# Optimization experiments

Measured on AMD Instinct MI355X. Metric: run time of the kernel, lower is better.

The kernel has to match this reference:

```python
import jax, jax.numpy as jnp
import numpy as np


def _sample_level(tables, gx, gy, align_corners):
    # tables: [3, C, H, W]; gx, gy: [3, P] grid coords in [-1, 1]
    # emulates F.grid_sample(mode='bilinear', padding_mode='border')
    def one(tab, x, y):
        C, H, W = tab.shape
        if align_corners:
            ix = (x + 1.0) * 0.5 * (W - 1)
            iy = (y + 1.0) * 0.5 * (H - 1)
        else:
            ix = ((x + 1.0) * W - 1.0) * 0.5
            iy = ((y + 1.0) * H - 1.0) * 0.5
        ix = jnp.clip(ix, 0.0, W - 1.0)  # border padding
        iy = jnp.clip(iy, 0.0, H - 1.0)
        x0 = jnp.floor(ix)
        y0 = jnp.floor(iy)
        wx = ix - x0
        wy = iy - y0
        x0i = x0.astype(jnp.int32)
        y0i = y0.astype(jnp.int32)
        x1i = jnp.minimum(x0i + 1, W - 1)
        y1i = jnp.minimum(y0i + 1, H - 1)
        v00 = tab[:, y0i, x0i]  # [C, P]
        v01 = tab[:, y0i, x1i]
        v10 = tab[:, y1i, x0i]
        v11 = tab[:, y1i, x1i]
        top = v00 * (1.0 - wx) + v01 * wx
        bot = v10 * (1.0 - wx) + v11 * wx
        return (top * (1.0 - wy) + bot * wy).T  # [P, C]

    return jax.vmap(one, in_axes=(0, 0, 0))(tables, gx, gy)  # [3, P, C]


def _hexplane(xyz, t, bounds, sps, tps):
    lead = xyz.shape[:-1]
    xyz = xyz.reshape(-1, 3)
    t = t.reshape(-1, t.shape[-1])
    xyzn = (xyz - bounds[:, 0, :]) / (bounds[:, 1, :] - bounds[:, 0, :])
    x, y, z = xyzn[:, 0], xyzn[:, 1], xyzn[:, 2]
    # spatial planes: xy, xz, yz; grid[...,0]->W, grid[...,1]->H
    sgx = jnp.stack([x, x, y]) * 2.0 - 1.0  # [3, P]
    sgy = jnp.stack([y, z, z]) * 2.0 - 1.0
    tt = t[:, 0]
    # temporal planes: (t, x), (t, y), (t, z); t -> W (dim_time), coord -> H (res)
    tgx = jnp.stack([tt, tt, tt]) * 2.0 - 1.0
    tgy = jnp.stack([x, y, z]) * 2.0 - 1.0
    sfeat = jnp.concatenate([_sample_level(sp, sgx, sgy, False) for sp in sps], axis=-1)  # [3, P, C*L]
    tfeat = jnp.concatenate([_sample_level(tp, tgx, tgy, True) for tp in tps], axis=-1)   # [3, P, C*L]
    feat = jnp.concatenate([sfeat, tfeat], axis=0)  # [6, P, C*L]
    val = jnp.transpose(feat, (1, 0, 2)).reshape(feat.shape[1], -1)  # [P, 6*C*L]
    return val.reshape(*lead, val.shape[-1])


def setup_inputs() -> dict:
    key = jax.random.key(0)
    N = 1_000_000
    C = 8
    T = 100
    STD = 0.1
    resolutions = [16, 32, 64, 128]
    ks = jax.random.split(key, 2 + 2 * len(resolutions))
    xyz = jax.random.uniform(ks[0], (N, 3), dtype=jnp.float32)
    t = jax.random.uniform(ks[1], (N, 1), dtype=jnp.float32)
    bounds = jnp.stack([jnp.zeros((1, 3), jnp.float32), jnp.ones((1, 3), jnp.float32)], axis=1)  # [1, 2, 3]
    inp = {"xyz": xyz, "t": t, "bounds": bounds}
    for i, r in enumerate(resolutions):
        inp[f"sp{i}"] = jax.random.uniform(ks[2 + i], (3, C, r, r), jnp.float32, -STD, STD)
        inp[f"tp{i}"] = jax.random.uniform(ks[2 + len(resolutions) + i], (3, C, r, T), jnp.float32, -STD, STD)
    return inp


def reference(xyz, t, bounds, sp0, sp1, sp2, sp3, tp0, tp1, tp2, tp3):
    return _hexplane(xyz, t, bounds, (sp0, sp1, sp2, sp3), (tp0, tp1, tp2, tp3))
```

## Files before the change

kernel.cpp:

```cpp
#include <hip/hip_runtime.h>
#include <hip/hip_bf16.h>

typedef float f32x2 __attribute__((ext_vector_type(2)));
typedef float f32x4 __attribute__((ext_vector_type(4)));
typedef unsigned int u32;
typedef u32 u32x4 __attribute__((ext_vector_type(4)));

#define Y_SP0 0
#define Y_SP1 13056
#define Y_SP2 63744
#define Y_TP0 263424
#define Y_TP1 340992
#define Y_TP2 496128
#define Y_TP3 806400
#define P_SP3 1426944

#define G 4

__global__ __launch_bounds__(256) void build_tabs(
    const float* __restrict__ sp0, const float* __restrict__ sp1,
    const float* __restrict__ sp2, const float* __restrict__ sp3,
    const float* __restrict__ tp0, const float* __restrict__ tp1,
    const float* __restrict__ tp2, const float* __restrict__ tp3,
    unsigned short* __restrict__ dst)
{
    int id = blockIdx.y;
    const float* src; int W, H, off; bool yp;
    switch (id) {
        case 0: src = sp0; W = 16;  H = 16;  off = Y_SP0; yp = true;  break;
        case 1: src = sp1; W = 32;  H = 32;  off = Y_SP1; yp = true;  break;
        case 2: src = sp2; W = 64;  H = 64;  off = Y_SP2; yp = true;  break;
        case 3: src = tp0; W = 100; H = 16;  off = Y_TP0; yp = true;  break;
        case 4: src = tp1; W = 100; H = 32;  off = Y_TP1; yp = true;  break;
        case 5: src = tp2; W = 100; H = 64;  off = Y_TP2; yp = true;  break;
        case 6: src = tp3; W = 100; H = 128; off = Y_TP3; yp = true;  break;
        default:src = sp3; W = 128; H = 128; off = P_SP3; yp = false; break;
    }
    int HW = W * H;
    int i = blockIdx.x * 256 + threadIdx.x;
    float v;
    if (yp) {
        int Wp = W + 1;
        int total = 3 * H * Wp * 16;
        if (i >= total) return;
        int half = i & 1;
        int c    = (i >> 1) & 7;
        int q    = i >> 4;
        int x  = q % Wp;
        int y  = (q / Wp) % H;
        int pl = q / (H * Wp);
        int xs = min(x, W - 1);
        int ys = half ? min(y + 1, H - 1) : y;
        v = src[(size_t)(pl * 8 + c) * HW + (size_t)ys * W + xs];
    } else {
        int total = 3 * HW * 8;
        if (i >= total) return;
        int c = i & 7;
        int q = i >> 3;
        int x  = q % W;
        int y  = (q / W) % H;
        int pl = q / HW;
        v = src[(size_t)(pl * 8 + c) * HW + (size_t)y * W + x];
    }
    __hip_bfloat16 b = __float2bfloat16(v);
    dst[off + i] = *reinterpret_cast<unsigned short*>(&b);
}

__device__ __forceinline__ float dot2bf(u32 ab, u32 w, float acc) {
    float d;
    asm("v_dot2_f32_bf16 %0, %1, %2, %3" : "=v"(d) : "v"(ab), "v"(w), "v"(acc));
    return d;
}
__device__ __forceinline__ u32 pk_bf16(float lo, float hi) {
    u32 d;
    asm("v_cvt_pk_bf16_f32 %0, %1, %2" : "=v"(d) : "v"(lo), "v"(hi));
    return d;
}

__global__ __launch_bounds__(192) void hexplane_pipe(
    const float* __restrict__ xyz, const float* __restrict__ t,
    const float* __restrict__ bounds, const unsigned short* __restrict__ tw,
    float* __restrict__ out, int N)
{
    __shared__ float coords[3][8][4];
    __shared__ f32x4 lutA[24];
    __shared__ f32x4 lutB[24];
    __shared__ float ostage[1536];

    int tid   = threadIdx.x;
    int gbase = blockIdx.x * (G * 8);

    if (tid < 64) {
        int grp = tid >> 5, pp = (tid >> 2) & 7, comp = tid & 3;
        int n = gbase + grp * 8 + pp;
        float v = 0.0f;
        if (n < N) {
            if (comp < 3) {
                float b0 = bounds[comp], b1 = bounds[3 + comp];
                v = (xyz[(size_t)n * 3 + comp] - b0) / (b1 - b0);
            } else {
                v = t[n];
            }
        }
        coords[grp][pp][comp] = v;
    } else if (tid < 88) {
        int pos = tid - 64;
        int s = (pos < 9) ? pos + pos / 3 : (pos < 21) ? pos + 3 : 4 * (pos - 21) + 3;
        int g = s >> 2;
        int r = s & 3;
        int res = 16 << r;
        bool plain = (g < 3) && (r == 3);
        float sx, ox, sy, oy, cx, cy;
        int base_u, Ws, selx, sely;
        if (g < 3) {
            sx = (float)res; ox = -0.5f;
            sy = (float)res; oy = -0.5f;
            cx = (float)(res - 1); cy = (float)(res - 1);
            selx = (g == 2) ? 1 : 0;
            sely = (g == 0) ? 1 : 2;
            if (plain) {
                Ws = 128;
                base_u = P_SP3 + g * 128 * 128 * 8;
            } else {
                Ws = res + 1;
                int lo = (r == 0) ? Y_SP0 : (r == 1) ? Y_SP1 : Y_SP2;
                base_u = lo + g * res * (res + 1) * 16;
            }
        } else {
            int q = g - 3;
            Ws = 101;
            sx = 99.0f; ox = 0.0f;
            sy = (float)(res - 1); oy = 0.0f;
            cx = 99.0f; cy = (float)(res - 1);
            int lo = (r == 0) ? Y_TP0 : (r == 1) ? Y_TP1 : (r == 2) ? Y_TP2 : Y_TP3;
            base_u = lo + q * res * 101 * 16;
            selx = 3;
            sely = q;
        }
        int code = Ws | (selx << 9) | (sely << 12) | (plain ? (1 << 15) : 0) | (s << 16);
        f32x4 A = { sx, ox, sy, oy };
        f32x4 B = { cx, cy, __int_as_float(base_u * 2), __int_as_float(code) };
        lutA[pos] = A;
        lutB[pos] = B;
    }
    __syncthreads();

    int p   = tid & 7;
    int pos = tid >> 3;

    f32x4 A = lutA[pos];
    f32x4 B = lutB[pos];
    int code  = __float_as_int(B[3]);
    int Ws    = code & 511;
    int selx  = (code >> 9) & 7;
    int sely  = (code >> 12) & 7;
    bool plain = (code >> 15) & 1;
    int s     = (code >> 16) & 31;
    const char* tb = (const char*)tw + __float_as_int(B[2]);

    int e   = p * 24 + s;
    int k_w = p & 1;
    float* bw0 = &ostage[e * 8 + (k_w ? 4 : 0)];
    float* bw1 = &ostage[e * 8 + (k_w ? 0 : 4)];

    int e0 = tid >> 1, a0 = tid & 1;
    int p0 = (e0 * 683) >> 14;
    const float* rd0 = &ostage[e0 * 8 + (a0 ^ (p0 & 1)) * 4];
    int m1 = tid + 192;
    int e1 = m1 >> 1, a1 = m1 & 1;
    int p1 = (e1 * 683) >> 14;
    const float* rd1 = &ostage[e1 * 8 + (a1 ^ (p1 & 1)) * 4];

    u32 wA, wB_;
    u32x4 L0, L1, L2, L3;

    auto PREP = [&](int q) {
        int cb = q % 3;
        float fx = coords[cb][p][selx];
        float fy = coords[cb][p][sely];
        float ix = fmaf(fx, A[0], A[1]);
        float iy = fmaf(fy, A[2], A[3]);
        ix = fminf(fmaxf(ix, 0.0f), B[0]);
        iy = fminf(fmaxf(iy, 0.0f), B[1]);
        float x0f = floorf(ix), y0f = floorf(iy);
        float wx = ix - x0f, wy = iy - y0f;
        int x0 = (int)x0f, y0 = (int)y0f;
        float omx = 1.0f - wx, omy = 1.0f - wy;
        if (!plain) {
            wA  = pk_bf16(omx * omy, omx * wy);
            wB_ = pk_bf16(wx * omy,  wx * wy);
            const char* ad = tb + (size_t)(y0 * Ws + x0) * 32;
            L0 = *(const u32x4*)(ad);
            L1 = *(const u32x4*)(ad + 16);
            L2 = *(const u32x4*)(ad + 32);
            L3 = *(const u32x4*)(ad + 48);
        } else {
            wA  = pk_bf16(omx * omy, wx * omy);
            wB_ = pk_bf16(omx * wy,  wx * wy);
            int x1 = min(x0 + 1, 127), y1 = min(y0 + 1, 127);
            L0 = *(const u32x4*)(tb + (size_t)(y0 * 128 + x0) * 16);
            L1 = *(const u32x4*)(tb + (size_t)(y0 * 128 + x1) * 16);
            L2 = *(const u32x4*)(tb + (size_t)(y1 * 128 + x0) * 16);
            L3 = *(const u32x4*)(tb + (size_t)(y1 * 128 + x1) * 16);
        }
    };

    PREP(0);

    size_t total_out = (size_t)N * 192;
    size_t outbase   = (size_t)blockIdx.x * (G * 1536);

    for (int g = 0; g < G; ++g) {
        float f[8];
        if (!plain) {
            #pragma unroll
            for (int k = 0; k < 4; ++k) {
                f[k]     = dot2bf(L2[k], wB_, dot2bf(L0[k], wA, 0.0f));
                f[4 + k] = dot2bf(L3[k], wB_, dot2bf(L1[k], wA, 0.0f));
            }
        } else {
            #pragma unroll
            for (int k = 0; k < 4; ++k) {
                u32 tA2 = __builtin_amdgcn_perm(L0[k], L1[k], 0x01000504u);
                u32 tB2 = __builtin_amdgcn_perm(L0[k], L1[k], 0x03020706u);
                u32 bA2 = __builtin_amdgcn_perm(L2[k], L3[k], 0x01000504u);
                u32 bB2 = __builtin_amdgcn_perm(L2[k], L3[k], 0x03020706u);
                f[2*k]     = dot2bf(bA2, wB_, dot2bf(tA2, wA, 0.0f));
                f[2*k + 1] = dot2bf(bB2, wB_, dot2bf(tB2, wA, 0.0f));
            }
        }

        if (g + 1 < G) PREP(g + 1);

        *(f32x4*)bw0 = *(f32x4*)&f[0];
        *(f32x4*)bw1 = *(f32x4*)&f[4];

        float vc = 0.0f;
        bool doc = (g + 2 < G) && (tid < 32);
        if (doc) {
            int comp = tid & 3;
            int n = gbase + (g + 2) * 8 + (tid >> 2);
            if (n < N) {
                if (comp < 3) {
                    float b0 = bounds[comp], b1 = bounds[3 + comp];
                    vc = (xyz[(size_t)n * 3 + comp] - b0) / (b1 - b0);
                } else {
                    vc = t[n];
                }
            }
        }

        __syncthreads();

        f32x4 v0 = *(const f32x4*)rd0;
        f32x4 v1 = *(const f32x4*)rd1;
        size_t F0 = outbase + (size_t)g * 1536 + (size_t)tid * 4;
        size_t F1 = F0 + 768;
        if (F0 + 4 <= total_out)
            __builtin_nontemporal_store(v0, (f32x4*)(out + F0));
        if (F1 + 4 <= total_out)
            __builtin_nontemporal_store(v1, (f32x4*)(out + F1));

        if (doc) coords[(g + 2) % 3][tid >> 2][tid & 3] = vc;

        __syncthreads();
    }
}

extern "C" void kernel_launch(void* const* d_in, const int* in_sizes, int n_in,
                              void* d_out, int out_size, void* d_ws, size_t ws_size,
                              hipStream_t stream) {
    const float* xyz    = (const float*)d_in[0];
    const float* t      = (const float*)d_in[1];
    const float* bounds = (const float*)d_in[2];
    const float* sp[4]  = { (const float*)d_in[3], (const float*)d_in[5],
                            (const float*)d_in[7], (const float*)d_in[9] };
    const float* tp[4]  = { (const float*)d_in[4], (const float*)d_in[6],
                            (const float*)d_in[8], (const float*)d_in[10] };
    float* out = (float*)d_out;

    int N = in_sizes[0] / 3;
    unsigned short* tw = (unsigned short*)d_ws;

    build_tabs<<<dim3(2424, 8), 256, 0, stream>>>(
        sp[0], sp[1], sp[2], sp[3], tp[0], tp[1], tp[2], tp[3], tw);

    int blocks = (N + G * 8 - 1) / (G * 8);
    hexplane_pipe<<<blocks, 192, 0, stream>>>(xyz, t, bounds, tw, out, N);
}
```

Measured before the change: 222.9 us.

## Double-buffer output staging to drop a barrier and double points per block

Doubles the shared-memory output staging buffer so each loop iteration needs one __syncthreads instead of two. The prefetched coordinate write moves ahead of the barrier. Also doubles the number of groups per block (G 4→8), switches table addressing to 32-bit offsets, and hoists the output bounds check into one per-block flag. Fewer barriers and amortised setup should let the store-bound loop run more smoothly, at the cost of more shared memory per block and half as many blocks.

```diff
diff --git a/kernel.cpp b/kernel.cpp
--- a/kernel.cpp
+++ b/kernel.cpp
@@ -15,7 +15,7 @@
 #define Y_TP3 806400
 #define P_SP3 1426944
 
-#define G 4
+#define G 8
 
 __global__ __launch_bounds__(256) void build_tabs(
     const float* __restrict__ sp0, const float* __restrict__ sp1,
@@ -77,7 +77,7 @@
     return d;
 }
 
-__global__ __launch_bounds__(192) void hexplane_pipe(
+__global__ __launch_bounds__(192) void hexplane_pipe2(
     const float* __restrict__ xyz, const float* __restrict__ t,
     const float* __restrict__ bounds, const unsigned short* __restrict__ tw,
     float* __restrict__ out, int N)
@@ -85,7 +85,7 @@
     __shared__ float coords[3][8][4];
     __shared__ f32x4 lutA[24];
     __shared__ f32x4 lutB[24];
-    __shared__ float ostage[1536];
+    __shared__ float ostage[2][1536];
 
     int tid   = threadIdx.x;
     int gbase = blockIdx.x * (G * 8);
@@ -156,20 +156,21 @@
     int sely  = (code >> 12) & 7;
     bool plain = (code >> 15) & 1;
     int s     = (code >> 16) & 31;
-    const char* tb = (const char*)tw + __float_as_int(B[2]);
+    u32 base_byte = (u32)__float_as_int(B[2]);
+    const char* twb = (const char*)tw;
 
     int e   = p * 24 + s;
     int k_w = p & 1;
-    float* bw0 = &ostage[e * 8 + (k_w ? 4 : 0)];
-    float* bw1 = &ostage[e * 8 + (k_w ? 0 : 4)];
+    int bwo0 = e * 8 + (k_w ? 4 : 0);
+    int bwo1 = e * 8 + (k_w ? 0 : 4);
 
     int e0 = tid >> 1, a0 = tid & 1;
     int p0 = (e0 * 683) >> 14;
-    const float* rd0 = &ostage[e0 * 8 + (a0 ^ (p0 & 1)) * 4];
+    int rdo0 = e0 * 8 + (a0 ^ (p0 & 1)) * 4;
     int m1 = tid + 192;
     int e1 = m1 >> 1, a1 = m1 & 1;
     int p1 = (e1 * 683) >> 14;
-    const float* rd1 = &ostage[e1 * 8 + (a1 ^ (p1 & 1)) * 4];
+    int rdo1 = e1 * 8 + (a1 ^ (p1 & 1)) * 4;
 
     u32 wA, wB_;
     u32x4 L0, L1, L2, L3;
@@ -189,19 +190,19 @@
         if (!plain) {
             wA  = pk_bf16(omx * omy, omx * wy);
             wB_ = pk_bf16(wx * omy,  wx * wy);
-            const char* ad = tb + (size_t)(y0 * Ws + x0) * 32;
-            L0 = *(const u32x4*)(ad);
-            L1 = *(const u32x4*)(ad + 16);
-            L2 = *(const u32x4*)(ad + 32);
-            L3 = *(const u32x4*)(ad + 48);
+            u32 off = base_byte + (u32)(y0 * Ws + x0) * 32;
+            L0 = *(const u32x4*)(twb + off);
+            L1 = *(const u32x4*)(twb + off + 16);
+            L2 = *(const u32x4*)(twb + off + 32);
+            L3 = *(const u32x4*)(twb + off + 48);
         } else {
             wA  = pk_bf16(omx * omy, wx * omy);
             wB_ = pk_bf16(omx * wy,  wx * wy);
             int x1 = min(x0 + 1, 127), y1 = min(y0 + 1, 127);
-            L0 = *(const u32x4*)(tb + (size_t)(y0 * 128 + x0) * 16);
-            L1 = *(const u32x4*)(tb + (size_t)(y0 * 128 + x1) * 16);
-            L2 = *(const u32x4*)(tb + (size_t)(y1 * 128 + x0) * 16);
-            L3 = *(const u32x4*)(tb + (size_t)(y1 * 128 + x1) * 16);
+            L0 = *(const u32x4*)(twb + base_byte + (u32)(y0 * 128 + x0) * 16);
+            L1 = *(const u32x4*)(twb + base_byte + (u32)(y0 * 128 + x1) * 16);
+            L2 = *(const u32x4*)(twb + base_byte + (u32)(y1 * 128 + x0) * 16);
+            L3 = *(const u32x4*)(twb + base_byte + (u32)(y1 * 128 + x1) * 16);
         }
     };
 
@@ -209,6 +210,7 @@
 
     size_t total_out = (size_t)N * 192;
     size_t outbase   = (size_t)blockIdx.x * (G * 1536);
+    bool safe = (outbase + (size_t)G * 1536) <= total_out;
 
     for (int g = 0; g < G; ++g) {
         float f[8];
@@ -232,14 +234,14 @@
 
         if (g + 1 < G) PREP(g + 1);
 
-        *(f32x4*)bw0 = *(f32x4*)&f[0];
-        *(f32x4*)bw1 = *(f32x4*)&f[4];
-
-        float vc = 0.0f;
-        bool doc = (g + 2 < G) && (tid < 32);
-        if (doc) {
+        float* ob = ostage[g & 1];
+        *(f32x4*)&ob[bwo0] = *(f32x4*)&f[0];
+        *(f32x4*)&ob[bwo1] = *(f32x4*)&f[4];
+
+        if ((g + 2 < G) && (tid < 32)) {
             int comp = tid & 3;
             int n = gbase + (g + 2) * 8 + (tid >> 2);
+            float vc = 0.0f;
             if (n < N) {
                 if (comp < 3) {
                     float b0 = bounds[comp], b1 = bounds[3 + comp];
@@ -248,22 +250,24 @@
                     vc = t[n];
                 }
             }
+            coords[(g + 2) % 3][tid >> 2][comp] = vc;
         }
 
         __syncthreads();
 
-        f32x4 v0 = *(const f32x4*)rd0;
-        f32x4 v1 = *(const f32x4*)rd1;
+        f32x4 v0 = *(const f32x4*)&ob[rdo0];
+        f32x4 v1 = *(const f32x4*)&ob[rdo1];
         size_t F0 = outbase + (size_t)g * 1536 + (size_t)tid * 4;
         size_t F1 = F0 + 768;
-        if (F0 + 4 <= total_out)
+        if (safe) {
             __builtin_nontemporal_store(v0, (f32x4*)(out + F0));
-        if (F1 + 4 <= total_out)
             __builtin_nontemporal_store(v1, (f32x4*)(out + F1));
-
-        if (doc) coords[(g + 2) % 3][tid >> 2][tid & 3] = vc;
-
-        __syncthreads();
+        } else {
+            if (F0 + 4 <= total_out)
+                __builtin_nontemporal_store(v0, (f32x4*)(out + F0));
+            if (F1 + 4 <= total_out)
+                __builtin_nontemporal_store(v1, (f32x4*)(out + F1));
+        }
     }
 }
 
@@ -286,5 +290,5 @@
         sp[0], sp[1], sp[2], sp[3], tp[0], tp[1], tp[2], tp[3], tw);
 
     int blocks = (N + G * 8 - 1) / (G * 8);
-    hexplane_pipe<<<blocks, 192, 0, stream>>>(xyz, t, bounds, tw, out, N);
-}
+    hexplane_pipe2<<<blocks, 192, 0, stream>>>(xyz, t, bounds, tw, out, N);
+}
```

Result: slower. 257.9 us (+15.7%).
